# Kernel optimization log

Measured on AMD Instinct MI355X. Metric: run time of the kernel, lower is better.

Reference implementation:

```python
import jax, jax.numpy as jnp
import numpy as np

B, S, D, C, H = 4, 2048, 1024, 2, 16
LN_EPS = 1e-5


def setup_inputs() -> dict:
    key = jax.random.key(0)
    ks = jax.random.split(key, 6)
    return {
        "token_emb": jax.random.normal(ks[0], (B, S, D), dtype=jnp.float32),
        "chunk_w": jax.random.normal(ks[1], (D, C * D), dtype=jnp.float32) * 0.02,
        "chunk_b": jnp.zeros((D,), dtype=jnp.float32),
        "in_proj_w": jax.random.normal(ks[2], (3 * D, D), dtype=jnp.float32) * 0.02,
        "in_proj_b": jnp.zeros((3 * D,), dtype=jnp.float32),
        "out_proj_w": jax.random.normal(ks[3], (D, D), dtype=jnp.float32) * 0.02,
        "out_proj_b": jnp.zeros((D,), dtype=jnp.float32),
        "ln_g": jnp.ones((D,), dtype=jnp.float32),
        "ln_b": jnp.zeros((D,), dtype=jnp.float32),
        "num_heads": H,
    }


def _layer_norm(x, g, b):
    mu = jnp.mean(x, axis=-1, keepdims=True)
    var = jnp.mean((x - mu) ** 2, axis=-1, keepdims=True)
    return (x - mu) * jax.lax.rsqrt(var + LN_EPS) * g + b


def reference(token_emb, chunk_w, chunk_b, in_proj_w, in_proj_b,
              out_proj_w, out_proj_b, ln_g, ln_b, num_heads):
    Bq, Sq, Dq = token_emb.shape
    c = chunk_w.shape[1] // Dq
    # Sliding windows with zero padding at the end (vectorized unfold).
    padded = jnp.pad(token_emb, ((0, 0), (0, c - 1), (0, 0)))
    # (B, S, c*D): concat the c shifted views along feature dim
    windows = jnp.concatenate([padded[:, k:k + Sq, :] for k in range(c)], axis=-1)
    chunk = jnp.einsum('bsf,df->bsd', windows, chunk_w) + chunk_b  # (B,S,D)

    # Multi-head self-attention (torch nn.MultiheadAttention semantics).
    qkv = jnp.einsum('bsd,ed->bse', chunk, in_proj_w) + in_proj_b
    q, k, v = jnp.split(qkv, 3, axis=-1)
    dh = Dq // num_heads
    q = q.reshape(Bq, Sq, num_heads, dh)
    k = k.reshape(Bq, Sq, num_heads, dh)
    v = v.reshape(Bq, Sq, num_heads, dh)
    scores = jnp.einsum('bqhd,bkhd->bhqk', q, k) / jnp.sqrt(jnp.float32(dh))
    probs = jax.nn.softmax(scores, axis=-1)
    attn = jnp.einsum('bhqk,bkhd->bqhd', probs, v).reshape(Bq, Sq, Dq)
    attn = jnp.einsum('bsd,ed->bse', attn, out_proj_w) + out_proj_b

    return _layer_norm(chunk + attn, ln_g, ln_b)
```

## Files before the change

kernel.cpp:

```cpp
#include <hip/hip_runtime.h>


typedef __bf16 bf16x8 __attribute__((ext_vector_type(8)));
typedef float f32x4 __attribute__((ext_vector_type(4)));
typedef float f32x16 __attribute__((ext_vector_type(16)));

#if __has_builtin(__builtin_amdgcn_exp2f)
#define EXP2(x) __builtin_amdgcn_exp2f(x)
#else
#define EXP2(x) exp2f(x)
#endif

__device__ __forceinline__ unsigned short f2bf(float x) {
  unsigned u = __float_as_uint(x);
  u += 0x7fffu + ((u >> 16) & 1u);
  return (unsigned short)(u >> 16);
}

__device__ __forceinline__ float bf2f(unsigned short x) {
  return __uint_as_float(((unsigned)x) << 16);
}

__device__ __forceinline__ void glds16(const ushort* g, ushort* l) {
  __builtin_amdgcn_global_load_lds(
      (const __attribute__((address_space(1))) unsigned int*)g,
      (__attribute__((address_space(3))) unsigned int*)l, 16, 0, 0);
}

__global__ __launch_bounds__(256) void cvt_emb(const float* __restrict__ emb,
                                               ushort* __restrict__ embb) {
  const int i = blockIdx.x * 256 + threadIdx.x;
  const int e = i * 4;
  const int m = e >> 10;
  const int b = m >> 11, s = m & 2047;
  float4 v = *(const float4*)(emb + (size_t)e);
  ushort4 o;
  o.x = f2bf(v.x); o.y = f2bf(v.y); o.z = f2bf(v.z); o.w = f2bf(v.w);
  *(ushort4*)(embb + ((size_t)(b * 2049 + s) << 10) + (e & 1023)) = o;
}

__global__ void zrow_kernel(ushort* __restrict__ embb) {
  const int b = blockIdx.x, t = threadIdx.x;
  ushort4 z = {0, 0, 0, 0};
  *(ushort4*)(embb + ((size_t)(b * 2049 + 2048) << 10) + t * 4) = z;
}

__global__ __launch_bounds__(256) void cvt_bf16(const float* __restrict__ in,
                                                ushort* __restrict__ out, int n4) {
  const int i = blockIdx.x * 256 + threadIdx.x;
  if (i >= n4) return;
  float4 v = ((const float4*)in)[i];
  ushort4 o;
  o.x = f2bf(v.x); o.y = f2bf(v.y); o.z = f2bf(v.z); o.w = f2bf(v.w);
  ((ushort4*)out)[i] = o;
}

__global__ __launch_bounds__(256) void gemm_chunk(
    const ushort* __restrict__ embb, const ushort* __restrict__ cwb,
    const float* __restrict__ bias, ushort* __restrict__ outb) {
  __shared__ __align__(16) ushort sA[8192];
  __shared__ __align__(16) ushort sA2[512];
  __shared__ __align__(16) ushort sB1[4096];
  __shared__ __align__(16) ushort sB2[4096];
  const int t = threadIdx.x, wave = t >> 6, lane = t & 63;
  const int c16 = lane & 15, quad = lane >> 4;
  const int wm = wave >> 1, wn = wave & 1;
  const int m0 = blockIdx.x * 128, n0 = blockIdx.y * 64;
  const int b = m0 >> 11, s0 = m0 & 2047;
  const size_t rowbase = (size_t)(b * 2049 + s0);
  f32x4 acc[4][2] = {};
  const ushort* gA[4];
  ushort* lA[4];
#pragma unroll
  for (int c = 0; c < 4; ++c) {
    const int j = wave * 4 + c;
    const int ks = j >> 1, row = (j & 1) * 64 + lane;
    gA[c] = embb + ((rowbase + row) << 10) + ks * 8;
    lA[c] = sA + j * 512;
  }
  const ushort* gA2 = embb + ((rowbase + 128) << 10) + (lane & 7) * 8;
  const ushort* gB1[2];
  const ushort* gB2[2];
  ushort* lB1[2];
  ushort* lB2[2];
#pragma unroll
  for (int c = 0; c < 2; ++c) {
    const int j = wave * 2 + c;
    gB1[c] = cwb + (size_t)(n0 + lane) * 2048 + j * 8;
    gB2[c] = gB1[c] + 1024;
    lB1[c] = sB1 + j * 512;
    lB2[c] = sB2 + j * 512;
  }
  for (int k0 = 0; k0 < 1024; k0 += 64) {
    __syncthreads();
#pragma unroll
    for (int c = 0; c < 4; ++c) glds16(gA[c] + k0, lA[c]);
    if (wave == 3) glds16(gA2 + k0, sA2);
#pragma unroll
    for (int c = 0; c < 2; ++c) {
      glds16(gB1[c] + k0, lB1[c]);
      glds16(gB2[c] + k0, lB2[c]);
    }
    __syncthreads();
#pragma unroll
    for (int kc = 0; kc < 2; ++kc) {
      const int ksl = kc * 4 + quad;
      bf16x8 af1[4], af2[4], bf1[2], bf2[2];
#pragma unroll
      for (int i = 0; i < 4; ++i) {
        const int row = wm * 64 + i * 16 + c16;
        af1[i] = *(const bf16x8*)(sA + (ksl * 128 + row) * 8);
        const ushort* p2 = (row + 1 < 128) ? (sA + (ksl * 128 + row + 1) * 8)
                                           : (sA2 + ksl * 8);
        af2[i] = *(const bf16x8*)p2;
      }
#pragma unroll
      for (int i = 0; i < 2; ++i) {
        bf1[i] = *(const bf16x8*)(sB1 + (ksl * 64 + wn * 32 + i * 16 + c16) * 8);
        bf2[i] = *(const bf16x8*)(sB2 + (ksl * 64 + wn * 32 + i * 16 + c16) * 8);
      }
#pragma unroll
      for (int mt = 0; mt < 4; ++mt)
#pragma unroll
        for (int nt = 0; nt < 2; ++nt) {
          acc[mt][nt] = __builtin_amdgcn_mfma_f32_16x16x32_bf16(af1[mt], bf1[nt],
                                                                acc[mt][nt], 0, 0, 0);
          acc[mt][nt] = __builtin_amdgcn_mfma_f32_16x16x32_bf16(af2[mt], bf2[nt],
                                                                acc[mt][nt], 0, 0, 0);
        }
    }
  }
  float bv[2];
#pragma unroll
  for (int nt = 0; nt < 2; ++nt) bv[nt] = bias[n0 + wn * 32 + nt * 16 + c16];
#pragma unroll
  for (int mt = 0; mt < 4; ++mt)
#pragma unroll
    for (int nt = 0; nt < 2; ++nt) {
      const int n = n0 + wn * 32 + nt * 16 + c16;
#pragma unroll
      for (int r = 0; r < 4; ++r) {
        const int m = m0 + wm * 64 + mt * 16 + quad * 4 + r;
        outb[(size_t)m * 1024 + n] = f2bf(acc[mt][nt][r] + bv[nt]);
      }
    }
}

template <int NT>
__global__ __launch_bounds__(256) void gemm_bt(
    const ushort* __restrict__ A, const ushort* __restrict__ W,
    const float* __restrict__ bias, int M, int N, int K, int mode,
    float* __restrict__ outf, ushort* __restrict__ outb,
    const ushort* __restrict__ residb) {
  constexpr int NTC = NT / 32;
  constexpr int BC  = NT / 32;
  __shared__ __align__(16) ushort sA[8192];
  __shared__ __align__(16) ushort sB[NT * 64];
  const int t = threadIdx.x, wave = t >> 6, lane = t & 63;
  const int c16 = lane & 15, quad = lane >> 4;
  const int wm = wave >> 1, wn = wave & 1;
  const int m0 = blockIdx.x * 128, n0 = blockIdx.y * NT;
  f32x4 acc[4][NTC] = {};
  const ushort* gA[4];
  const ushort* gB[BC];
  ushort* lA[4];
  ushort* lB[BC];
#pragma unroll
  for (int c = 0; c < 4; ++c) {
    const int j = wave * 4 + c;
    const int ks = j >> 1, row = (j & 1) * 64 + lane;
    gA[c] = A + (size_t)(m0 + row) * K + ks * 8;
    lA[c] = sA + j * 512;
  }
#pragma unroll
  for (int c = 0; c < BC; ++c) {
    const int j = wave * BC + c;
    int ksb, rowb;
    if (NT == 128) { ksb = j >> 1; rowb = (j & 1) * 64 + lane; }
    else           { ksb = j;      rowb = lane; }
    gB[c] = W + (size_t)(n0 + rowb) * K + ksb * 8;
    lB[c] = sB + j * 512;
  }
  for (int k0 = 0; k0 < K; k0 += 64) {
    __syncthreads();
#pragma unroll
    for (int c = 0; c < 4; ++c) glds16(gA[c] + k0, lA[c]);
#pragma unroll
    for (int c = 0; c < BC; ++c) glds16(gB[c] + k0, lB[c]);
    __syncthreads();
#pragma unroll
    for (int kc = 0; kc < 2; ++kc) {
      bf16x8 af[4], bfr[NTC];
#pragma unroll
      for (int i = 0; i < 4; ++i)
        af[i] = *(const bf16x8*)(sA + ((kc * 4 + quad) * 128 + wm * 64 + i * 16 + c16) * 8);
#pragma unroll
      for (int i = 0; i < NTC; ++i)
        bfr[i] = *(const bf16x8*)(sB + ((kc * 4 + quad) * NT + wn * (NT / 2) + i * 16 + c16) * 8);
#pragma unroll
      for (int mt = 0; mt < 4; ++mt)
#pragma unroll
        for (int nt = 0; nt < NTC; ++nt)
          acc[mt][nt] = __builtin_amdgcn_mfma_f32_16x16x32_bf16(af[mt], bfr[nt],
                                                                acc[mt][nt], 0, 0, 0);
    }
  }
  const float QS = 0.18033688011112042f;
  float bv[NTC];
#pragma unroll
  for (int nt = 0; nt < NTC; ++nt) bv[nt] = bias[n0 + wn * (NT / 2) + nt * 16 + c16];
#pragma unroll
  for (int mt = 0; mt < 4; ++mt) {
#pragma unroll
    for (int nt = 0; nt < NTC; ++nt) {
      const int n = n0 + wn * (NT / 2) + nt * 16 + c16;
#pragma unroll
      for (int r = 0; r < 4; ++r) {
        const int m = m0 + wm * 64 + mt * 16 + quad * 4 + r;
        const size_t idx = (size_t)m * N + n;
        float v = acc[mt][nt][r] + bv[nt];
        if (mode == 2)      { outf[idx] = v + bf2f(residb[idx]); }
        else {
          if (n < 1024) v *= QS;
          outb[idx] = f2bf(v);
        }
      }
    }
  }
}

__global__ __launch_bounds__(256) void vtrans(const ushort* __restrict__ qkv,
                                              ushort* __restrict__ vt) {
  const int sb = blockIdx.x, h = blockIdx.y, b = blockIdx.z;
  __shared__ ushort tile[64][72];
  const int t = threadIdx.x;
  {
    const int row = t >> 3, c8 = (t & 7) * 8;
    const ushort* src = qkv + (size_t)(b * 2048 + sb * 64 + row) * 3072 + 2048 + h * 64 + c8;
    *(uint4*)&tile[row][c8]      = *(const uint4*)src;
    *(uint4*)&tile[row + 32][c8] = *(const uint4*)(src + 32 * 3072);
  }
  __syncthreads();
  const int d = t >> 2, seg = (t & 3) * 16;
  unsigned wbuf[8];
#pragma unroll
  for (int i = 0; i < 8; ++i)
    wbuf[i] = (unsigned)tile[seg + 2 * i][d] | ((unsigned)tile[seg + 2 * i + 1][d] << 16);
  ushort* dst = vt + (size_t)((b * 16 + h) * 64 + d) * 2048 + sb * 64 + seg;
  uint4 oA = make_uint4(wbuf[0], wbuf[1], wbuf[4], wbuf[5]);
  uint4 oB = make_uint4(wbuf[2], wbuf[3], wbuf[6], wbuf[7]);
  *(uint4*)(dst)     = oA;
  *(uint4*)(dst + 8) = oB;
}

__global__ __launch_bounds__(256, 4) void attn_kernel(
    const ushort* __restrict__ qkv, const ushort* __restrict__ vtp,
    ushort* __restrict__ attn_out) {
  const int S = 2048;
  const int bh = blockIdx.x, qblk = blockIdx.y;
  const int h = bh & 15, b = bh >> 4;
  const int t = threadIdx.x, wave = t >> 6, lane = t & 63;
  const int c32 = lane & 31, hi = lane >> 5;
  __shared__ __align__(16) ushort sK[8192];
  __shared__ __align__(16) ushort sV[8192];
  const int q0 = qblk * 128;
  const size_t qrow = (size_t)(b * S + q0 + wave * 32 + c32);
  const int swv0 = (c32 ^ (c32 >> 3)) & 15;
  const int dv1 = 32 + c32;
  const int swv1 = (dv1 ^ (dv1 >> 3)) & 15;
  bf16x8 qf[4];
  {
    const ushort* qp = qkv + qrow * 3072 + h * 64 + hi * 8;
#pragma unroll
    for (int dk = 0; dk < 4; ++dk) qf[dk] = *(const bf16x8*)(qp + dk * 16);
  }
  f32x16 o0 = {}, o1 = {};
  float li = 0.f;
  const int j0 = wave * 4;

  for (int kv0 = 0; kv0 < S; kv0 += 128) {
    __syncthreads();
#pragma unroll
    for (int c = 0; c < 4; ++c) {
      const int j = j0 + c;
      const int dslot = j >> 1, key = (j & 1) * 64 + lane;
      glds16(qkv + (size_t)(b * S + kv0 + key) * 3072 + 1024 + h * 64 + dslot * 8,
             sK + j * 512);
      const int d = j * 4 + (lane >> 4);
      const int ksv = (lane & 15) ^ ((d ^ (d >> 3)) & 15);
      glds16(vtp + (size_t)((b * 16 + h) * 64 + d) * S + kv0 + ksv * 8,
             sV + j * 512);
    }
    __syncthreads();
#pragma unroll
    for (int kt = 0; kt < 4; ++kt) {
      f32x16 z = {};
#pragma unroll
      for (int dk = 0; dk < 4; ++dk) {
        bf16x8 kf = *(const bf16x8*)(sK + ((dk * 2 + hi) * 128 + kt * 32 + c32) * 8);
        z = __builtin_amdgcn_mfma_f32_32x32x16_bf16(kf, qf[dk], z, 0, 0, 0);
      }
      uint2 w[4];
#pragma unroll
      for (int g = 0; g < 4; ++g) {
        const float p0 = EXP2(z[g * 4 + 0]);
        const float p1 = EXP2(z[g * 4 + 1]);
        const float p2 = EXP2(z[g * 4 + 2]);
        const float p3 = EXP2(z[g * 4 + 3]);
        li += (p0 + p1) + (p2 + p3);
        w[g].x = __builtin_amdgcn_perm(__float_as_uint(p1), __float_as_uint(p0),
                                       0x07060302u);
        w[g].y = __builtin_amdgcn_perm(__float_as_uint(p3), __float_as_uint(p2),
                                       0x07060302u);
      }
#pragma unroll
      for (int c = 0; c < 2; ++c) {
        const uint4 fr = make_uint4(w[2 * c].x, w[2 * c].y,
                                    w[2 * c + 1].x, w[2 * c + 1].y);
        bf16x8 pf;
        __builtin_memcpy(&pf, &fr, 16);
        const int ksl = kt * 4 + c * 2 + hi;
        bf16x8 vf0 = *(const bf16x8*)(sV + (c32 * 16 + (ksl ^ swv0)) * 8);
        o0 = __builtin_amdgcn_mfma_f32_32x32x16_bf16(vf0, pf, o0, 0, 0, 0);
        bf16x8 vf1 = *(const bf16x8*)(sV + (dv1 * 16 + (ksl ^ swv1)) * 8);
        o1 = __builtin_amdgcn_mfma_f32_32x32x16_bf16(vf1, pf, o1, 0, 0, 0);
      }
    }
  }
  li += __shfl_xor(li, 32);
  const float inv = 1.f / li;
  ushort* orow = attn_out + qrow * 1024 + h * 64;
#pragma unroll
  for (int dt = 0; dt < 2; ++dt) {
    const f32x16 ov = dt ? o1 : o0;
#pragma unroll
    for (int g = 0; g < 4; ++g) {
      float v0 = ov[g * 4 + 0] * inv, v1 = ov[g * 4 + 1] * inv;
      float v2 = ov[g * 4 + 2] * inv, v3 = ov[g * 4 + 3] * inv;
      uint2 w2;
      w2.x = (unsigned)f2bf(v0) | ((unsigned)f2bf(v1) << 16);
      w2.y = (unsigned)f2bf(v2) | ((unsigned)f2bf(v3) << 16);
      *(uint2*)(orow + dt * 32 + g * 8 + hi * 4) = w2;
    }
  }
}

__global__ __launch_bounds__(256) void ln_kernel(const float* __restrict__ y,
                                                 const float* __restrict__ g,
                                                 const float* __restrict__ bta,
                                                 float* __restrict__ out) {
  const int m = blockIdx.x;
  const int t = threadIdx.x;
  const float* row = y + (size_t)m * 1024;
  float4 v = ((const float4*)row)[t];
  float s = v.x + v.y + v.z + v.w;
  float s2 = v.x * v.x + v.y * v.y + v.z * v.z + v.w * v.w;
#pragma unroll
  for (int off = 1; off < 64; off <<= 1) {
    s += __shfl_xor(s, off, 64);
    s2 += __shfl_xor(s2, off, 64);
  }
  __shared__ float red[8];
  const int wave = t >> 6, lane = t & 63;
  if (lane == 0) { red[wave] = s; red[4 + wave] = s2; }
  __syncthreads();
  s = red[0] + red[1] + red[2] + red[3];
  s2 = red[4] + red[5] + red[6] + red[7];
  const float mu = s * (1.f / 1024.f);
  const float var = s2 * (1.f / 1024.f) - mu * mu;
  const float rs = rsqrtf(var + 1e-5f);
  float4 gg = ((const float4*)g)[t];
  float4 bb = ((const float4*)bta)[t];
  float4 o;
  o.x = (v.x - mu) * rs * gg.x + bb.x;
  o.y = (v.y - mu) * rs * gg.y + bb.y;
  o.z = (v.z - mu) * rs * gg.z + bb.z;
  o.w = (v.w - mu) * rs * gg.w + bb.w;
  ((float4*)(out + (size_t)m * 1024))[t] = o;
}

extern "C" void kernel_launch(void* const* d_in, const int* in_sizes, int n_in,
                              void* d_out, int out_size, void* d_ws, size_t ws_size,
                              hipStream_t stream) {
  const float* emb        = (const float*)d_in[0];
  const float* chunk_w    = (const float*)d_in[1];
  const float* chunk_b    = (const float*)d_in[2];
  const float* in_proj_w  = (const float*)d_in[3];
  const float* in_proj_b  = (const float*)d_in[4];
  const float* out_proj_w = (const float*)d_in[5];
  const float* out_proj_b = (const float*)d_in[6];
  const float* ln_g       = (const float*)d_in[7];
  const float* ln_b       = (const float*)d_in[8];

  char* w = (char*)d_ws;
  const size_t MBy = (size_t)1 << 20;
  ushort* embb   = (ushort*)(w + 0);
  ushort* qkvb   = (ushort*)(w + 17 * MBy);
  float*  y      = (float*)(w + 17 * MBy);
  ushort* chunkb = (ushort*)(w + 65 * MBy);
  ushort* vtb    = (ushort*)(w + 81 * MBy);
  ushort* attnb  = (ushort*)(w + 97 * MBy);
  ushort* cwb    = (ushort*)(w + 113 * MBy);
  ushort* ipwb   = (ushort*)(w + 117 * MBy);
  ushort* opwb   = (ushort*)(w + 123 * MBy);

  cvt_emb<<<8192, 256, 0, stream>>>(emb, embb);
  zrow_kernel<<<4, 256, 0, stream>>>(embb);
  cvt_bf16<<<2048, 256, 0, stream>>>(chunk_w, cwb, 2 * 1024 * 1024 / 4);
  cvt_bf16<<<3072, 256, 0, stream>>>(in_proj_w, ipwb, 3 * 1024 * 1024 / 4);
  cvt_bf16<<<1024, 256, 0, stream>>>(out_proj_w, opwb, 1024 * 1024 / 4);

  gemm_chunk<<<dim3(8192 / 128, 1024 / 64), 256, 0, stream>>>(
      embb, cwb, chunk_b, chunkb);

  gemm_bt<128><<<dim3(8192 / 128, 3072 / 128), 256, 0, stream>>>(
      chunkb, ipwb, in_proj_b, 8192, 3072, 1024, 1, nullptr, qkvb, nullptr);

  vtrans<<<dim3(32, 16, 4), 256, 0, stream>>>(qkvb, vtb);

  attn_kernel<<<dim3(64, 2048 / 128, 1), 256, 0, stream>>>(qkvb, vtb, attnb);

  gemm_bt<64><<<dim3(8192 / 128, 1024 / 64), 256, 0, stream>>>(
      attnb, opwb, out_proj_b, 8192, 1024, 1024, 2, y, nullptr, chunkb);

  ln_kernel<<<8192, 256, 0, stream>>>(y, ln_g, ln_b, (float*)d_out);
}
```

Baseline: 455.8 us.

## Fuse V transpose into QKV GEMM epilogue, merge conversions, store pre-LN output as bf16

```diff
diff --git a/kernel.cpp b/kernel.cpp
--- a/kernel.cpp
+++ b/kernel.cpp
@@ -27,32 +27,37 @@
       (__attribute__((address_space(3))) unsigned int*)l, 16, 0, 0);
 }
 
-__global__ __launch_bounds__(256) void cvt_emb(const float* __restrict__ emb,
-                                               ushort* __restrict__ embb) {
-  const int i = blockIdx.x * 256 + threadIdx.x;
-  const int e = i * 4;
-  const int m = e >> 10;
-  const int b = m >> 11, s = m & 2047;
-  float4 v = *(const float4*)(emb + (size_t)e);
-  ushort4 o;
-  o.x = f2bf(v.x); o.y = f2bf(v.y); o.z = f2bf(v.z); o.w = f2bf(v.w);
-  *(ushort4*)(embb + ((size_t)(b * 2049 + s) << 10) + (e & 1023)) = o;
-}
-
-__global__ void zrow_kernel(ushort* __restrict__ embb) {
-  const int b = blockIdx.x, t = threadIdx.x;
-  ushort4 z = {0, 0, 0, 0};
-  *(ushort4*)(embb + ((size_t)(b * 2049 + 2048) << 10) + t * 4) = z;
-}
-
-__global__ __launch_bounds__(256) void cvt_bf16(const float* __restrict__ in,
-                                                ushort* __restrict__ out, int n4) {
-  const int i = blockIdx.x * 256 + threadIdx.x;
-  if (i >= n4) return;
-  float4 v = ((const float4*)in)[i];
-  ushort4 o;
-  o.x = f2bf(v.x); o.y = f2bf(v.y); o.z = f2bf(v.z); o.w = f2bf(v.w);
-  ((ushort4*)out)[i] = o;
+__global__ __launch_bounds__(256) void cvt_all(
+    const float* __restrict__ emb, const float* __restrict__ cw,
+    const float* __restrict__ ipw, const float* __restrict__ opw,
+    ushort* __restrict__ embb, ushort* __restrict__ cwb,
+    ushort* __restrict__ ipwb, ushort* __restrict__ opwb) {
+  const int blk = blockIdx.x, t = threadIdx.x;
+  if (blk < 8192) {
+    const int i = blk * 256 + t;
+    const int e = i * 4;
+    const int m = e >> 10;
+    const int b = m >> 11, s = m & 2047;
+    float4 v = *(const float4*)(emb + (size_t)e);
+    ushort4 o;
+    o.x = f2bf(v.x); o.y = f2bf(v.y); o.z = f2bf(v.z); o.w = f2bf(v.w);
+    *(ushort4*)(embb + ((size_t)(b * 2049 + s) << 10) + (e & 1023)) = o;
+  } else if (blk < 8196) {
+    const int b = blk - 8192;
+    ushort4 z = {0, 0, 0, 0};
+    *(ushort4*)(embb + ((size_t)(b * 2049 + 2048) << 10) + t * 4) = z;
+  } else {
+    const float* src;
+    ushort* dst;
+    int i;
+    if (blk < 10244)      { src = cw;  dst = cwb;  i = (blk - 8196) * 256 + t; }
+    else if (blk < 13316) { src = ipw; dst = ipwb; i = (blk - 10244) * 256 + t; }
+    else                  { src = opw; dst = opwb; i = (blk - 13316) * 256 + t; }
+    float4 v = ((const float4*)src)[i];
+    ushort4 o;
+    o.x = f2bf(v.x); o.y = f2bf(v.y); o.z = f2bf(v.z); o.w = f2bf(v.w);
+    ((ushort4*)dst)[i] = o;
+  }
 }
 
 __global__ __launch_bounds__(256) void gemm_chunk(
@@ -150,8 +155,8 @@
 __global__ __launch_bounds__(256) void gemm_bt(
     const ushort* __restrict__ A, const ushort* __restrict__ W,
     const float* __restrict__ bias, int M, int N, int K, int mode,
-    float* __restrict__ outf, ushort* __restrict__ outb,
-    const ushort* __restrict__ residb) {
+    ushort* __restrict__ outb, const ushort* __restrict__ residb,
+    ushort* __restrict__ vtb) {
   constexpr int NTC = NT / 32;
   constexpr int BC  = NT / 32;
   __shared__ __align__(16) ushort sA[8192];
@@ -214,43 +219,32 @@
 #pragma unroll
     for (int nt = 0; nt < NTC; ++nt) {
       const int n = n0 + wn * (NT / 2) + nt * 16 + c16;
-#pragma unroll
-      for (int r = 0; r < 4; ++r) {
-        const int m = m0 + wm * 64 + mt * 16 + quad * 4 + r;
-        const size_t idx = (size_t)m * N + n;
-        float v = acc[mt][nt][r] + bv[nt];
-        if (mode == 2)      { outf[idx] = v + bf2f(residb[idx]); }
-        else {
-          if (n < 1024) v *= QS;
-          outb[idx] = f2bf(v);
+      const int mb = m0 + wm * 64 + mt * 16 + quad * 4;
+      if (mode == 2) {
+#pragma unroll
+        for (int r = 0; r < 4; ++r) {
+          const size_t idx = (size_t)(mb + r) * N + n;
+          outb[idx] = f2bf(acc[mt][nt][r] + bv[nt] + bf2f(residb[idx]));
         }
-      }
-    }
-  }
-}
-
-__global__ __launch_bounds__(256) void vtrans(const ushort* __restrict__ qkv,
-                                              ushort* __restrict__ vt) {
-  const int sb = blockIdx.x, h = blockIdx.y, b = blockIdx.z;
-  __shared__ ushort tile[64][72];
-  const int t = threadIdx.x;
-  {
-    const int row = t >> 3, c8 = (t & 7) * 8;
-    const ushort* src = qkv + (size_t)(b * 2048 + sb * 64 + row) * 3072 + 2048 + h * 64 + c8;
-    *(uint4*)&tile[row][c8]      = *(const uint4*)src;
-    *(uint4*)&tile[row + 32][c8] = *(const uint4*)(src + 32 * 3072);
-  }
-  __syncthreads();
-  const int d = t >> 2, seg = (t & 3) * 16;
-  unsigned wbuf[8];
-#pragma unroll
-  for (int i = 0; i < 8; ++i)
-    wbuf[i] = (unsigned)tile[seg + 2 * i][d] | ((unsigned)tile[seg + 2 * i + 1][d] << 16);
-  ushort* dst = vt + (size_t)((b * 16 + h) * 64 + d) * 2048 + sb * 64 + seg;
-  uint4 oA = make_uint4(wbuf[0], wbuf[1], wbuf[4], wbuf[5]);
-  uint4 oB = make_uint4(wbuf[2], wbuf[3], wbuf[6], wbuf[7]);
-  *(uint4*)(dst)     = oA;
-  *(uint4*)(dst + 8) = oB;
+      } else if (n < 2048) {
+        const float sc = (n < 1024) ? QS : 1.f;
+#pragma unroll
+        for (int r = 0; r < 4; ++r)
+          outb[(size_t)(mb + r) * 2048 + n] = f2bf((acc[mt][nt][r] + bv[nt]) * sc);
+      } else {
+        const int d = n - 2048, h = d >> 6, dd = d & 63;
+        const int b = mb >> 11, s = mb & 2047;
+        const int blk2 = (s >> 2) & 3;
+        const int sp = (blk2 == 1 || blk2 == 2) ? (s ^ 12) : s;
+        uint2 w2;
+        w2.x = (unsigned)f2bf(acc[mt][nt][0] + bv[nt]) |
+               ((unsigned)f2bf(acc[mt][nt][1] + bv[nt]) << 16);
+        w2.y = (unsigned)f2bf(acc[mt][nt][2] + bv[nt]) |
+               ((unsigned)f2bf(acc[mt][nt][3] + bv[nt]) << 16);
+        *(uint2*)(vtb + (size_t)((b * 16 + h) * 64 + dd) * 2048 + sp) = w2;
+      }
+    }
+  }
 }
 
 __global__ __launch_bounds__(256, 4) void attn_kernel(
@@ -270,7 +264,7 @@
   const int swv1 = (dv1 ^ (dv1 >> 3)) & 15;
   bf16x8 qf[4];
   {
-    const ushort* qp = qkv + qrow * 3072 + h * 64 + hi * 8;
+    const ushort* qp = qkv + qrow * 2048 + h * 64 + hi * 8;
 #pragma unroll
     for (int dk = 0; dk < 4; ++dk) qf[dk] = *(const bf16x8*)(qp + dk * 16);
   }
@@ -284,7 +278,7 @@
     for (int c = 0; c < 4; ++c) {
       const int j = j0 + c;
       const int dslot = j >> 1, key = (j & 1) * 64 + lane;
-      glds16(qkv + (size_t)(b * S + kv0 + key) * 3072 + 1024 + h * 64 + dslot * 8,
+      glds16(qkv + (size_t)(b * S + kv0 + key) * 2048 + 1024 + h * 64 + dslot * 8,
              sK + j * 512);
       const int d = j * 4 + (lane >> 4);
       const int ksv = (lane & 15) ^ ((d ^ (d >> 3)) & 15);
@@ -345,14 +339,15 @@
   }
 }
 
-__global__ __launch_bounds__(256) void ln_kernel(const float* __restrict__ y,
+__global__ __launch_bounds__(256) void ln_kernel(const ushort* __restrict__ yb,
                                                  const float* __restrict__ g,
                                                  const float* __restrict__ bta,
                                                  float* __restrict__ out) {
   const int m = blockIdx.x;
   const int t = threadIdx.x;
-  const float* row = y + (size_t)m * 1024;
-  float4 v = ((const float4*)row)[t];
+  const ushort4 u = ((const ushort4*)(yb + (size_t)m * 1024))[t];
+  float4 v;
+  v.x = bf2f(u.x); v.y = bf2f(u.y); v.z = bf2f(u.z); v.w = bf2f(u.w);
   float s = v.x + v.y + v.z + v.w;
   float s2 = v.x * v.x + v.y * v.y + v.z * v.z + v.w * v.w;
 #pragma unroll
@@ -396,32 +391,27 @@
   const size_t MBy = (size_t)1 << 20;
   ushort* embb   = (ushort*)(w + 0);
   ushort* qkvb   = (ushort*)(w + 17 * MBy);
-  float*  y      = (float*)(w + 17 * MBy);
-  ushort* chunkb = (ushort*)(w + 65 * MBy);
-  ushort* vtb    = (ushort*)(w + 81 * MBy);
-  ushort* attnb  = (ushort*)(w + 97 * MBy);
-  ushort* cwb    = (ushort*)(w + 113 * MBy);
-  ushort* ipwb   = (ushort*)(w + 117 * MBy);
-  ushort* opwb   = (ushort*)(w + 123 * MBy);
-
-  cvt_emb<<<8192, 256, 0, stream>>>(emb, embb);
-  zrow_kernel<<<4, 256, 0, stream>>>(embb);
-  cvt_bf16<<<2048, 256, 0, stream>>>(chunk_w, cwb, 2 * 1024 * 1024 / 4);
-  cvt_bf16<<<3072, 256, 0, stream>>>(in_proj_w, ipwb, 3 * 1024 * 1024 / 4);
-  cvt_bf16<<<1024, 256, 0, stream>>>(out_proj_w, opwb, 1024 * 1024 / 4);
+  ushort* yb     = (ushort*)(w + 17 * MBy);
+  ushort* chunkb = (ushort*)(w + 49 * MBy);
+  ushort* vtb    = (ushort*)(w + 65 * MBy);
+  ushort* attnb  = (ushort*)(w + 81 * MBy);
+  ushort* cwb    = (ushort*)(w + 97 * MBy);
+  ushort* ipwb   = (ushort*)(w + 101 * MBy);
+  ushort* opwb   = (ushort*)(w + 107 * MBy);
+
+  cvt_all<<<14340, 256, 0, stream>>>(emb, chunk_w, in_proj_w, out_proj_w,
+                                     embb, cwb, ipwb, opwb);
 
   gemm_chunk<<<dim3(8192 / 128, 1024 / 64), 256, 0, stream>>>(
       embb, cwb, chunk_b, chunkb);
 
   gemm_bt<128><<<dim3(8192 / 128, 3072 / 128), 256, 0, stream>>>(
-      chunkb, ipwb, in_proj_b, 8192, 3072, 1024, 1, nullptr, qkvb, nullptr);
-
-  vtrans<<<dim3(32, 16, 4), 256, 0, stream>>>(qkvb, vtb);
+      chunkb, ipwb, in_proj_b, 8192, 3072, 1024, 1, qkvb, nullptr, vtb);
 
   attn_kernel<<<dim3(64, 2048 / 128, 1), 256, 0, stream>>>(qkvb, vtb, attnb);
 
   gemm_bt<64><<<dim3(8192 / 128, 1024 / 64), 256, 0, stream>>>(
-      attnb, opwb, out_proj_b, 8192, 1024, 1024, 2, y, nullptr, chunkb);
-
-  ln_kernel<<<8192, 256, 0, stream>>>(y, ln_g, ln_b, (float*)d_out);
-}
+      attnb, opwb, out_proj_b, 8192, 1024, 1024, 2, yb, chunkb, nullptr);
+
+  ln_kernel<<<8192, 256, 0, stream>>>(yb, ln_g, ln_b, (float*)d_out);
+}
```

New measurement: 427.5 us. 6.2% less time.
